# Performance work log

Hardware: AMD Instinct MI355X
Metric: run time of the kernel (lower is better)

The kernel has to match this reference:

```python
import jax, jax.numpy as jnp
import numpy as np

N_HEAD = 8
DROP_RATE = 0.1


def setup_inputs() -> dict:
    key = jax.random.key(0)
    k1, k2, k3 = jax.random.split(key, 3)
    n, c, h, w = 16, 512, 32, 32
    return {
        "x": jax.random.normal(k1, (n, c, h, w), jnp.float32),
        "qkv_w": jax.random.normal(k2, (3 * c, c), jnp.float32) * 0.02,
        "qkv_b": jnp.zeros((3 * c,), jnp.float32),
        "out_w": jax.random.normal(k3, (c, c), jnp.float32) * 0.02,
        "out_b": jnp.zeros((c,), jnp.float32),
        "dropout_enabled": 0,
    }


def reference(x, qkv_w, qkv_b, out_w, out_b, dropout_enabled):
    n, c, h, w = x.shape
    hd = c // N_HEAD  # head dim
    # fused QKV 1x1 conv == per-pixel matmul: [n, 3c, h, w]
    qkv = jnp.einsum('oc,nchw->nohw', qkv_w, x) + qkv_b[None, :, None, None]
    # [n, 3*n_head, hd, h*w] -> [n, 3*n_head, h*w, hd]
    qkv = jnp.swapaxes(qkv.reshape(n, N_HEAD * 3, hd, h * w), 2, 3)
    q, k, v = jnp.split(qkv, 3, axis=1)  # each [n, n_head, hw, hd]
    scale = hd ** (-0.25)
    att = jax.nn.softmax((q * scale) @ (jnp.swapaxes(k, 2, 3) * scale), axis=3)
    y = jnp.swapaxes(att @ v, 2, 3).reshape(n, c, h, w)
    y = jnp.einsum('oc,nchw->nohw', out_w, y) + out_b[None, :, None, None]
    # Dropout2d: drops whole (n, c) channel maps
    rate = DROP_RATE * dropout_enabled
    keep = jax.random.bernoulli(jax.random.key(42), 1.0 - rate, shape=(n, c))
    y = y * keep[..., None, None] / (1.0 - rate)
    return x + y
```

## Files before the change

### kernel.cpp

```cpp
#include <hip/hip_runtime.h>

typedef short bf16x8 __attribute__((ext_vector_type(8)));
typedef float f32x4 __attribute__((ext_vector_type(4)));
typedef float f32x16 __attribute__((ext_vector_type(16)));

#define MFMA16(a,b,c) __builtin_amdgcn_mfma_f32_16x16x32_bf16((a),(b),(c),0,0,0)
#define MFMA32(a,b,c) __builtin_amdgcn_mfma_f32_32x32x16_bf16((a),(b),(c),0,0,0)

static __device__ __forceinline__ unsigned short f2bf(float f){
  unsigned u; __builtin_memcpy(&u, &f, 4);
  u += 0x7fffu + ((u >> 16) & 1u);
  return (unsigned short)(u >> 16);
}

static __device__ __forceinline__ unsigned cvtpk(float lo, float hi){
  unsigned r;
  asm volatile("v_cvt_pk_bf16_f32 %0, %1, %2" : "=v"(r) : "v"(lo), "v"(hi));
  return r;
}
static __device__ __forceinline__ void pl32swap(unsigned &a, unsigned &b){
  asm volatile("v_permlane32_swap_b32 %0, %1" : "+v"(a), "+v"(b));
}

static __device__ __forceinline__ void gload_lds16(const void* g, void* l) {
  __builtin_amdgcn_global_load_lds(
      (__attribute__((address_space(1))) void*)g,
      (__attribute__((address_space(3))) void*)l, 16, 0, 0);
}

__global__ __launch_bounds__(256) void cvt_bf16(
    const float* __restrict__ in, unsigned short* __restrict__ out, int n) {
  int i = blockIdx.x * 256 + threadIdx.x;
  if (i < n) out[i] = f2bf(in[i]);
}

__global__ __launch_bounds__(256) void transpose_cvt(
    const float* __restrict__ in, unsigned short* __restrict__ out)
{
  __shared__ unsigned short tile[32][33];
  const long base = (long)blockIdx.z * 512 * 1024;
  const int t = threadIdx.x, tx = t & 31, ty = t >> 5;
  const int c0 = blockIdx.x * 32, r0 = blockIdx.y * 32;
  const float* ib = in + base;
#pragma unroll
  for (int i = 0; i < 4; ++i)
    tile[ty + i * 8][tx] = f2bf(ib[(long)(r0 + ty + i * 8) * 1024 + c0 + tx]);
  __syncthreads();
  unsigned short* ob = out + base;
#pragma unroll
  for (int i = 0; i < 4; ++i)
    ob[(long)(c0 + ty + i * 8) * 512 + r0 + tx] = tile[tx][ty + i * 8];
}

__global__ __launch_bounds__(256, 2) void gemm_qkv(
    const unsigned short* __restrict__ A, const unsigned short* __restrict__ B,
    unsigned short* __restrict__ qkvout, const float* __restrict__ bias)
{
  const int M = 1024, K = 512;
  __shared__ unsigned short SM[4][128 * 64];
  const int t = threadIdx.x, lane = t & 63, wv = t >> 6;
  const int quad = lane >> 4, ln = lane & 15;

  const int L = blockIdx.x + 12 * blockIdx.y + 96 * blockIdx.z;
  const int v = (L & 7) * 192 + (L >> 3);
  const int m0 = ((v / 12) & 7) * 128, n0 = (v % 12) * 128;
  const long zb = v / 96;
  A += zb * (long)M * K;

  const int srow = wv * 32 + (lane >> 3);
  const int scol = ((lane & 7) * 8) ^ ((lane >> 3) * 8);

  auto stage = [&](int kt, unsigned short* Ad, unsigned short* Bd) {
#pragma unroll
    for (int i = 0; i < 4; ++i) {
      gload_lds16(&A[(long)(m0 + srow + i * 8) * K + kt + scol],
                  &Ad[(wv * 32 + i * 8) * 64]);
      gload_lds16(&B[(long)(n0 + srow + i * 8) * K + kt + scol],
                  &Bd[(wv * 32 + i * 8) * 64]);
    }
  };

  f32x4 zero = {0.f, 0.f, 0.f, 0.f};
  f32x4 acc[4][4];
#pragma unroll
  for (int i = 0; i < 4; ++i)
#pragma unroll
    for (int j = 0; j < 4; ++j) acc[i][j] = zero;

  const int wm = (wv & 1) * 64, wn = (wv >> 1) * 64;
  const int rsw = (ln & 7) * 8;

  stage(0, SM[0], SM[2]);
  __syncthreads();
  for (int kt8 = 0; kt8 < 8; ++kt8) {
    const int cur = kt8 & 1;
    if (kt8 < 7) stage((kt8 + 1) * 64, SM[cur ^ 1], SM[2 + (cur ^ 1)]);
    const unsigned short* As = SM[cur];
    const unsigned short* Bs = SM[2 + cur];
#pragma unroll
    for (int kk = 0; kk < 64; kk += 32) {
      bf16x8 a[4], b[4];
#pragma unroll
      for (int i = 0; i < 4; ++i)
        a[i] = *(const bf16x8*)&As[(wm + i * 16 + ln) * 64 + ((kk + quad * 8) ^ rsw)];
#pragma unroll
      for (int j = 0; j < 4; ++j)
        b[j] = *(const bf16x8*)&Bs[(wn + j * 16 + ln) * 64 + ((kk + quad * 8) ^ rsw)];
#pragma unroll
      for (int i = 0; i < 4; ++i)
#pragma unroll
        for (int j = 0; j < 4; ++j)
          acc[i][j] = MFMA16(a[i], b[j], acc[i][j]);
    }
    __syncthreads();
  }

  const int part = n0 >> 9;
  if (part < 2) {
    const float qs = (part == 0) ? 0.18033688f : 1.0f;
    unsigned short (*T)[136] = (unsigned short(*)[136])&SM[0][0];
#pragma unroll
    for (int j = 0; j < 4; ++j) {
      const int oo = wn + j * 16 + ln;
      const float bb = bias[n0 + oo];
#pragma unroll
      for (int i = 0; i < 4; ++i) {
        const int pp = wm + i * 16 + quad * 4;
        f32x4 vv = acc[i][j];
#pragma unroll
        for (int r = 0; r < 4; ++r)
          T[pp + r][oo] = f2bf((vv[r] + bb) * qs);
      }
    }
    __syncthreads();
    unsigned short* qb = qkvout + (long)part * 8388608;
#pragma unroll
    for (int it = 0; it < 8; ++it) {
      const int idx = it * 256 + t;
      const int p = idx >> 4, c0 = (idx & 15) * 8;
      const int og = n0 + c0;
      const int h = (og >> 6) & 7, d = og & 63;
      bf16x8 val = *(const bf16x8*)&T[p][c0];
      *(bf16x8*)&qb[((long)(zb * 8 + h) * 1024 + m0 + p) * 64 + d] = val;
    }
  } else {
#pragma unroll
    for (int j = 0; j < 4; ++j) {
      const int o = n0 + wn + j * 16 + ln;
      const float bb = bias[o];
#pragma unroll
      for (int i = 0; i < 4; ++i) {
        const int p = m0 + wm + i * 16 + quad * 4;
        const long cidx = ((long)zb * 512 + (o - 1024)) * 1024 + p;
        f32x4 vv = acc[i][j];
        ushort4 st;
        st.x = f2bf(vv[0] + bb); st.y = f2bf(vv[1] + bb);
        st.z = f2bf(vv[2] + bb); st.w = f2bf(vv[3] + bb);
        *(ushort4*)&qkvout[16777216 + cidx] = st;
      }
    }
  }
}

__global__ __launch_bounds__(256, 2) void gemm_out(
    const unsigned short* __restrict__ A, const unsigned short* __restrict__ B,
    float* __restrict__ C, const float* __restrict__ bias,
    const float* __restrict__ xin, const int* __restrict__ de_ptr)
{
  const int M = 1024, K = 512;
  __shared__ unsigned short SM[4][128 * 64];
  const int t = threadIdx.x, lane = t & 63, wv = t >> 6;
  const int quad = lane >> 4, ln = lane & 15;

  const int L = blockIdx.x + 4 * blockIdx.y + 32 * blockIdx.z;
  const int v = (L & 7) * 64 + (L >> 3);
  const int m0 = ((v >> 2) & 7) * 128, n0 = (v & 3) * 128;
  const long zb = v >> 5;
  A += zb * (long)M * K;
  C += zb * 512l * M;
  xin += zb * 512l * M;

  const int srow = wv * 32 + (lane >> 3);
  const int scol = ((lane & 7) * 8) ^ ((lane >> 3) * 8);

  auto stage = [&](int kt, unsigned short* Ad, unsigned short* Bd) {
#pragma unroll
    for (int i = 0; i < 4; ++i) {
      gload_lds16(&A[(long)(m0 + srow + i * 8) * K + kt + scol],
                  &Ad[(wv * 32 + i * 8) * 64]);
      gload_lds16(&B[(long)(n0 + srow + i * 8) * K + kt + scol],
                  &Bd[(wv * 32 + i * 8) * 64]);
    }
  };

  f32x4 zero = {0.f, 0.f, 0.f, 0.f};
  f32x4 acc[4][4];
#pragma unroll
  for (int i = 0; i < 4; ++i)
#pragma unroll
    for (int j = 0; j < 4; ++j) acc[i][j] = zero;

  const int wm = (wv & 1) * 64, wn = (wv >> 1) * 64;
  const int rsw = (ln & 7) * 8;

  stage(0, SM[0], SM[2]);
  __syncthreads();
  for (int kt8 = 0; kt8 < 8; ++kt8) {
    const int cur = kt8 & 1;
    if (kt8 < 7) stage((kt8 + 1) * 64, SM[cur ^ 1], SM[2 + (cur ^ 1)]);
    const unsigned short* As = SM[cur];
    const unsigned short* Bs = SM[2 + cur];
#pragma unroll
    for (int kk = 0; kk < 64; kk += 32) {
      bf16x8 a[4], b[4];
#pragma unroll
      for (int i = 0; i < 4; ++i)
        a[i] = *(const bf16x8*)&As[(wm + i * 16 + ln) * 64 + ((kk + quad * 8) ^ rsw)];
#pragma unroll
      for (int j = 0; j < 4; ++j)
        b[j] = *(const bf16x8*)&Bs[(wn + j * 16 + ln) * 64 + ((kk + quad * 8) ^ rsw)];
#pragma unroll
      for (int i = 0; i < 4; ++i)
#pragma unroll
        for (int j = 0; j < 4; ++j)
          acc[i][j] = MFMA16(a[i], b[j], acc[i][j]);
    }
    __syncthreads();
  }

  float dscale = 1.0f / (1.0f - 0.1f * (float)de_ptr[0]);

#pragma unroll
  for (int j = 0; j < 4; ++j) {
    int o = n0 + wn + j * 16 + ln;
    float bb = bias[o];
#pragma unroll
    for (int i = 0; i < 4; ++i) {
      int p = m0 + wm + i * 16 + quad * 4;
      long cidx = (long)o * M + p;
      f32x4 vv = acc[i][j];
      float4 rx = *(const float4*)&xin[cidx];
      float4 st;
      st.x = rx.x + (vv[0] + bb) * dscale;
      st.y = rx.y + (vv[1] + bb) * dscale;
      st.z = rx.z + (vv[2] + bb) * dscale;
      st.w = rx.w + (vv[3] + bb) * dscale;
      *(float4*)&C[cidx] = st;
    }
  }
}

__global__ __launch_bounds__(256, 2) void attn_kernel(
    const unsigned short* __restrict__ q_pd, const unsigned short* __restrict__ k_pd,
    const unsigned short* __restrict__ v_cp, unsigned short* __restrict__ y_pc)
{
  __shared__ unsigned short Ks[2][128 * 64];
  __shared__ unsigned short Vs[2][64 * 128];
  const int t = threadIdx.x, lane = t & 63, wv = t >> 6;
  const int l31 = lane & 31, bh8 = (lane >> 5) * 8;
  const int qt = blockIdx.y >> 5;
  const int nh = blockIdx.x * 32 + (blockIdx.y & 31);
  const int n = nh >> 3, h = nh & 7;
  const int q0 = qt * 256;

  bf16x8 qa[2][4];
#pragma unroll
  for (int qg = 0; qg < 2; ++qg) {
    const unsigned short* qb =
        q_pd + ((long)nh * 1024 + q0 + wv * 64 + qg * 32 + l31) * 64;
#pragma unroll
    for (int ds = 0; ds < 4; ++ds)
      qa[qg][ds] = *(const bf16x8*)(qb + ds * 16 + bh8);
  }

  f32x16 zacc;
#pragma unroll
  for (int r = 0; r < 16; ++r) zacc[r] = 0.f;
  f32x16 o_acc[2][2];
  o_acc[0][0] = zacc; o_acc[0][1] = zacc; o_acc[1][0] = zacc; o_acc[1][1] = zacc;
  float l_acc[2] = {0.f, 0.f};

  const unsigned short* kg0 = k_pd + (long)nh * 1024 * 64;
  const unsigned short* vg0 = v_cp + ((long)n * 512 + h * 64) * 1024;

  const int krow = lane >> 3;
  const int kcol = ((lane & 7) * 8) ^ ((lane >> 3) * 8);
  const int vrow = lane >> 4;
  const int rsw = (lane & 7) * 8;
  const int vrsw = (l31 & 15) * 8;

#pragma unroll
  for (int i = 0; i < 4; ++i) {
    const int vr = i * 4 + vrow;
    const int vcol = ((lane & 15) ^ vr) * 8;
    gload_lds16(kg0 + (long)(wv * 32 + i * 8 + krow) * 64 + kcol,
                &Ks[0][(wv * 32 + i * 8) * 64]);
    gload_lds16(vg0 + (long)(wv * 16 + vr) * 1024 + vcol,
                &Vs[0][(wv * 16 + i * 4) * 128]);
  }
  __syncthreads();

  union U { bf16x8 v; unsigned u[4]; };
  auto sm_pack = [&](const f32x16& sv, bf16x8* paq, float& lac) {
    float e[16];
#pragma unroll
    for (int r = 0; r < 16; ++r) e[r] = __builtin_amdgcn_exp2f(sv[r]);
    float ls = 0.f;
#pragma unroll
    for (int r = 0; r < 16; ++r) ls += e[r];
    lac += ls;
    unsigned pk4[4][2];
#pragma unroll
    for (int hh = 0; hh < 4; ++hh) {
      pk4[hh][0] = cvtpk(e[4 * hh + 0], e[4 * hh + 1]);
      pk4[hh][1] = cvtpk(e[4 * hh + 2], e[4 * hh + 3]);
    }
#pragma unroll
    for (int hk = 0; hk < 2; ++hk) {
      unsigned a0 = pk4[2 * hk + 1][0], b0 = pk4[2 * hk][0];
      unsigned a1 = pk4[2 * hk + 1][1], b1 = pk4[2 * hk][1];
      pl32swap(a0, b0); pl32swap(a1, b1);
      U u; u.u[0] = b0; u.u[1] = b1; u.u[2] = a0; u.u[3] = a1;
      paq[hk] = u.v;
    }
  };

  for (int c = 0; c < 8; ++c) {
    const int cur = c & 1;
    if (c < 7) {
      const unsigned short* kg = kg0 + (long)(c + 1) * 128 * 64;
      const unsigned short* vg = vg0 + (c + 1) * 128;
      unsigned short* KsD = Ks[cur ^ 1];
      unsigned short* VsD = Vs[cur ^ 1];
#pragma unroll
      for (int i = 0; i < 4; ++i) {
        const int vr = i * 4 + vrow;
        const int vcol = ((lane & 15) ^ vr) * 8;
        gload_lds16(kg + (long)(wv * 32 + i * 8 + krow) * 64 + kcol,
                    &KsD[(wv * 32 + i * 8) * 64]);
        gload_lds16(vg + (long)(wv * 16 + vr) * 1024 + vcol,
                    &VsD[(wv * 16 + i * 4) * 128]);
      }
    }
    const unsigned short* KsC = Ks[cur];
    const unsigned short* VsC = Vs[cur];

#pragma unroll
    for (int kgi = 0; kgi < 4; ++kgi) {
      f32x16 s0 = zacc, s1 = zacc;
      __builtin_amdgcn_s_setprio(1);
#pragma unroll
      for (int ds = 0; ds < 4; ++ds) {
        bf16x8 ka = *(const bf16x8*)&KsC[(kgi * 32 + l31) * 64 + ((ds * 16 + bh8) ^ rsw)];
        s0 = MFMA32(ka, qa[0][ds], s0);
        s1 = MFMA32(ka, qa[1][ds], s1);
      }
      __builtin_amdgcn_s_setprio(0);
      bf16x8 pa[2][2];
      sm_pack(s0, pa[0], l_acc[0]);
      sm_pack(s1, pa[1], l_acc[1]);
      __builtin_amdgcn_s_setprio(1);
#pragma unroll
      for (int dg = 0; dg < 2; ++dg)
#pragma unroll
        for (int hk = 0; hk < 2; ++hk) {
          bf16x8 va = *(const bf16x8*)
              &VsC[(dg * 32 + l31) * 128 + (((kgi * 2 + hk) * 16 + bh8) ^ vrsw)];
          o_acc[dg][0] = MFMA32(va, pa[0][hk], o_acc[dg][0]);
          o_acc[dg][1] = MFMA32(va, pa[1][hk], o_acc[dg][1]);
        }
      __builtin_amdgcn_s_setprio(0);
    }
    __syncthreads();
  }

#pragma unroll
  for (int qg = 0; qg < 2; ++qg) {
    float la = l_acc[qg];
    la += __shfl_xor(la, 32);
    float linv = 1.0f / la;
    const int q = q0 + wv * 64 + qg * 32 + l31;
    unsigned short* yb = y_pc + ((long)n * 1024 + q) * 512 + h * 64;
#pragma unroll
    for (int dg = 0; dg < 2; ++dg) {
      f32x16 o = o_acc[dg][qg];
#pragma unroll
      for (int rq = 0; rq < 4; ++rq) {
        int d0 = dg * 32 + rq * 8 + (bh8 >> 1);
        ushort4 st;
        st.x = f2bf(o[rq * 4 + 0] * linv);
        st.y = f2bf(o[rq * 4 + 1] * linv);
        st.z = f2bf(o[rq * 4 + 2] * linv);
        st.w = f2bf(o[rq * 4 + 3] * linv);
        *(ushort4*)&yb[d0] = st;
      }
    }
  }
}

extern "C" void kernel_launch(void* const* d_in, const int* in_sizes, int n_in,
                              void* d_out, int out_size, void* d_ws, size_t ws_size,
                              hipStream_t stream) {
  (void)in_sizes; (void)n_in; (void)out_size; (void)ws_size;
  const float* x     = (const float*)d_in[0];
  const float* qkv_w = (const float*)d_in[1];
  const float* qkv_b = (const float*)d_in[2];
  const float* out_w = (const float*)d_in[3];
  const float* out_b = (const float*)d_in[4];
  const int* de = (const int*)d_in[5];
  float* out = (float*)d_out;
  unsigned short* ws = (unsigned short*)d_ws;

  unsigned short* xT   = ws;
  unsigned short* qkv  = ws + 8388608;
  unsigned short* y_pc = ws;
  unsigned short* wq   = ws + 33554432;
  unsigned short* wo   = wq + 786432;

  cvt_bf16<<<3072, 256, 0, stream>>>(qkv_w, wq, 786432);
  cvt_bf16<<<1024, 256, 0, stream>>>(out_w, wo, 262144);

  transpose_cvt<<<dim3(32, 16, 16), 256, 0, stream>>>(x, xT);

  gemm_qkv<<<dim3(12, 8, 16), 256, 0, stream>>>(xT, wq, qkv, qkv_b);

  attn_kernel<<<dim3(4, 128), 256, 0, stream>>>(
      qkv, qkv + 8388608, qkv + 16777216, y_pc);

  gemm_out<<<dim3(4, 8, 16), 256, 0, stream>>>(
      y_pc, wo, out, out_b, x, de);
}
```

Before: 186.0 us.

## Split attention query tile across eight waves of 32 queries each

The attention block grows from 256 to 512 threads. Each wave now owns 32 query rows instead of 64, and the K/V staging into shared memory is divided among the eight waves. The aim is to raise wave-level parallelism and cut per-wave accumulator registers to improve latency hiding. In exchange, each K/V fragment read from LDS feeds only one MFMA instead of two, which doubles LDS read traffic. The stricter launch bound also caps registers tightly and may cause spills, while LDS usage of 64KB per block still limits how many blocks fit per CU.

New measurement: 187.7 us. Within noise of the previous version (+0.9%).

```diff
diff --git a/kernel.cpp b/kernel.cpp
--- a/kernel.cpp
+++ b/kernel.cpp
@@ -250,7 +250,7 @@
   }
 }
 
-__global__ __launch_bounds__(256, 2) void attn_kernel(
+__global__ __launch_bounds__(512, 4) void attn_kernel(
     const unsigned short* __restrict__ q_pd, const unsigned short* __restrict__ k_pd,
     const unsigned short* __restrict__ v_cp, unsigned short* __restrict__ y_pc)
 {
@@ -263,22 +263,21 @@
   const int n = nh >> 3, h = nh & 7;
   const int q0 = qt * 256;
 
-  bf16x8 qa[2][4];
-#pragma unroll
-  for (int qg = 0; qg < 2; ++qg) {
+  bf16x8 qa[4];
+  {
     const unsigned short* qb =
-        q_pd + ((long)nh * 1024 + q0 + wv * 64 + qg * 32 + l31) * 64;
+        q_pd + ((long)nh * 1024 + q0 + wv * 32 + l31) * 64;
 #pragma unroll
     for (int ds = 0; ds < 4; ++ds)
-      qa[qg][ds] = *(const bf16x8*)(qb + ds * 16 + bh8);
+      qa[ds] = *(const bf16x8*)(qb + ds * 16 + bh8);
   }
 
   f32x16 zacc;
 #pragma unroll
   for (int r = 0; r < 16; ++r) zacc[r] = 0.f;
-  f32x16 o_acc[2][2];
-  o_acc[0][0] = zacc; o_acc[0][1] = zacc; o_acc[1][0] = zacc; o_acc[1][1] = zacc;
-  float l_acc[2] = {0.f, 0.f};
+  f32x16 o_acc[2];
+  o_acc[0] = zacc; o_acc[1] = zacc;
+  float l_acc = 0.f;
 
   const unsigned short* kg0 = k_pd + (long)nh * 1024 * 64;
   const unsigned short* vg0 = v_cp + ((long)n * 512 + h * 64) * 1024;
@@ -289,26 +288,31 @@
   const int rsw = (lane & 7) * 8;
   const int vrsw = (l31 & 15) * 8;
 
-#pragma unroll
-  for (int i = 0; i < 4; ++i) {
-    const int vr = i * 4 + vrow;
-    const int vcol = ((lane & 15) ^ vr) * 8;
-    gload_lds16(kg0 + (long)(wv * 32 + i * 8 + krow) * 64 + kcol,
-                &Ks[0][(wv * 32 + i * 8) * 64]);
-    gload_lds16(vg0 + (long)(wv * 16 + vr) * 1024 + vcol,
-                &Vs[0][(wv * 16 + i * 4) * 128]);
-  }
+  auto stage_kv = [&](const unsigned short* kg, const unsigned short* vg,
+                      unsigned short* KsD, unsigned short* VsD) {
+#pragma unroll
+    for (int i = 0; i < 2; ++i) {
+      const int vr = ((wv & 1) * 8) + i * 4 + vrow;
+      const int vcol = ((lane & 15) ^ vr) * 8;
+      gload_lds16(kg + (long)(wv * 16 + i * 8 + krow) * 64 + kcol,
+                  &KsD[(wv * 16 + i * 8) * 64]);
+      gload_lds16(vg + (long)(wv * 8 + i * 4 + vrow) * 1024 + vcol,
+                  &VsD[(wv * 8 + i * 4) * 128]);
+    }
+  };
+
+  stage_kv(kg0, vg0, Ks[0], Vs[0]);
   __syncthreads();
 
   union U { bf16x8 v; unsigned u[4]; };
-  auto sm_pack = [&](const f32x16& sv, bf16x8* paq, float& lac) {
+  auto sm_pack = [&](const f32x16& sv, bf16x8* paq) {
     float e[16];
 #pragma unroll
     for (int r = 0; r < 16; ++r) e[r] = __builtin_amdgcn_exp2f(sv[r]);
     float ls = 0.f;
 #pragma unroll
     for (int r = 0; r < 16; ++r) ls += e[r];
-    lac += ls;
+    l_acc += ls;
     unsigned pk4[4][2];
 #pragma unroll
     for (int hh = 0; hh < 4; ++hh) {
@@ -327,38 +331,24 @@
 
   for (int c = 0; c < 8; ++c) {
     const int cur = c & 1;
-    if (c < 7) {
-      const unsigned short* kg = kg0 + (long)(c + 1) * 128 * 64;
-      const unsigned short* vg = vg0 + (c + 1) * 128;
-      unsigned short* KsD = Ks[cur ^ 1];
-      unsigned short* VsD = Vs[cur ^ 1];
-#pragma unroll
-      for (int i = 0; i < 4; ++i) {
-        const int vr = i * 4 + vrow;
-        const int vcol = ((lane & 15) ^ vr) * 8;
-        gload_lds16(kg + (long)(wv * 32 + i * 8 + krow) * 64 + kcol,
-                    &KsD[(wv * 32 + i * 8) * 64]);
-        gload_lds16(vg + (long)(wv * 16 + vr) * 1024 + vcol,
-                    &VsD[(wv * 16 + i * 4) * 128]);
-      }
-    }
+    if (c < 7)
+      stage_kv(kg0 + (long)(c + 1) * 128 * 64, vg0 + (c + 1) * 128,
+               Ks[cur ^ 1], Vs[cur ^ 1]);
     const unsigned short* KsC = Ks[cur];
     const unsigned short* VsC = Vs[cur];
 
 #pragma unroll
     for (int kgi = 0; kgi < 4; ++kgi) {
-      f32x16 s0 = zacc, s1 = zacc;
+      f32x16 s = zacc;
       __builtin_amdgcn_s_setprio(1);
 #pragma unroll
       for (int ds = 0; ds < 4; ++ds) {
         bf16x8 ka = *(const bf16x8*)&KsC[(kgi * 32 + l31) * 64 + ((ds * 16 + bh8) ^ rsw)];
-        s0 = MFMA32(ka, qa[0][ds], s0);
-        s1 = MFMA32(ka, qa[1][ds], s1);
+        s = MFMA32(ka, qa[ds], s);
       }
       __builtin_amdgcn_s_setprio(0);
-      bf16x8 pa[2][2];
-      sm_pack(s0, pa[0], l_acc[0]);
-      sm_pack(s1, pa[1], l_acc[1]);
+      bf16x8 pa[2];
+      sm_pack(s, pa);
       __builtin_amdgcn_s_setprio(1);
 #pragma unroll
       for (int dg = 0; dg < 2; ++dg)
@@ -366,24 +356,22 @@
         for (int hk = 0; hk < 2; ++hk) {
           bf16x8 va = *(const bf16x8*)
               &VsC[(dg * 32 + l31) * 128 + (((kgi * 2 + hk) * 16 + bh8) ^ vrsw)];
-          o_acc[dg][0] = MFMA32(va, pa[0][hk], o_acc[dg][0]);
-          o_acc[dg][1] = MFMA32(va, pa[1][hk], o_acc[dg][1]);
+          o_acc[dg] = MFMA32(va, pa[hk], o_acc[dg]);
         }
       __builtin_amdgcn_s_setprio(0);
     }
     __syncthreads();
   }
 
-#pragma unroll
-  for (int qg = 0; qg < 2; ++qg) {
-    float la = l_acc[qg];
+  {
+    float la = l_acc;
     la += __shfl_xor(la, 32);
     float linv = 1.0f / la;
-    const int q = q0 + wv * 64 + qg * 32 + l31;
+    const int q = q0 + wv * 32 + l31;
     unsigned short* yb = y_pc + ((long)n * 1024 + q) * 512 + h * 64;
 #pragma unroll
     for (int dg = 0; dg < 2; ++dg) {
-      f32x16 o = o_acc[dg][qg];
+      f32x16 o = o_acc[dg];
 #pragma unroll
       for (int rq = 0; rq < 4; ++rq) {
         int d0 = dg * 32 + rq * 8 + (bh8 >> 1);
@@ -424,7 +412,7 @@
 
   gemm_qkv<<<dim3(12, 8, 16), 256, 0, stream>>>(xT, wq, qkv, qkv_b);
 
-  attn_kernel<<<dim3(4, 128), 256, 0, stream>>>(
+  attn_kernel<<<dim3(4, 128), 512, 0, stream>>>(
       qkv, qkv + 8388608, qkv + 16777216, y_pc);
 
   gemm_out<<<dim3(4, 8, 16), 256, 0, stream>>>(
```

## Triple-buffer attention K/V with 512-thread blocks and split-wait pipelining in GEMMs

Applied to the files above, without the earlier changes.

The attention kernel moves to 512-thread blocks that each cover 512 queries, with K/V staging split across 8 waves. It triple-buffers the K/V tiles in LDS and prefetches two chunks ahead, using explicit vmcnt waits and raw barriers in place of full __syncthreads. Both GEMMs replace __syncthreads with a partial vmcnt wait plus s_barrier so the next tile's loads stay in flight, and the two weight-conversion launches are merged into one. The intent is more load/compute overlap and fewer launches, at the cost of more LDS per block (96KB), which may reduce occupancy. The hand-written vmcnt counts must match the number of outstanding loads exactly or reads become unsafe.

Result: slower. 198.8 us (+6.8%).

```diff
diff --git a/kernel.cpp b/kernel.cpp
--- a/kernel.cpp
+++ b/kernel.cpp
@@ -28,10 +28,12 @@
       (__attribute__((address_space(3))) void*)l, 16, 0, 0);
 }
 
-__global__ __launch_bounds__(256) void cvt_bf16(
-    const float* __restrict__ in, unsigned short* __restrict__ out, int n) {
+__global__ __launch_bounds__(256) void cvt_w(
+    const float* __restrict__ qkv_w, const float* __restrict__ out_w,
+    unsigned short* __restrict__ wq, unsigned short* __restrict__ wo) {
   int i = blockIdx.x * 256 + threadIdx.x;
-  if (i < n) out[i] = f2bf(in[i]);
+  if (i < 786432) wq[i] = f2bf(qkv_w[i]);
+  else            wo[i - 786432] = f2bf(out_w[i - 786432]);
 }
 
 __global__ __launch_bounds__(256) void transpose_cvt(
@@ -91,10 +93,15 @@
   const int rsw = (ln & 7) * 8;
 
   stage(0, SM[0], SM[2]);
-  __syncthreads();
   for (int kt8 = 0; kt8 < 8; ++kt8) {
     const int cur = kt8 & 1;
-    if (kt8 < 7) stage((kt8 + 1) * 64, SM[cur ^ 1], SM[2 + (cur ^ 1)]);
+    if (kt8 < 7) {
+      stage((kt8 + 1) * 64, SM[cur ^ 1], SM[2 + (cur ^ 1)]);
+      asm volatile("s_waitcnt vmcnt(8)" ::: "memory");
+    } else {
+      asm volatile("s_waitcnt vmcnt(0)" ::: "memory");
+    }
+    __builtin_amdgcn_s_barrier();
     const unsigned short* As = SM[cur];
     const unsigned short* Bs = SM[2 + cur];
 #pragma unroll
@@ -112,13 +119,14 @@
         for (int j = 0; j < 4; ++j)
           acc[i][j] = MFMA16(a[i], b[j], acc[i][j]);
     }
-    __syncthreads();
+    __builtin_amdgcn_s_barrier();
   }
 
   const int part = n0 >> 9;
   if (part < 2) {
     const float qs = (part == 0) ? 0.18033688f : 1.0f;
     unsigned short (*T)[136] = (unsigned short(*)[136])&SM[0][0];
+    __syncthreads();
 #pragma unroll
     for (int j = 0; j < 4; ++j) {
       const int oo = wn + j * 16 + ln;
@@ -204,10 +212,15 @@
   const int rsw = (ln & 7) * 8;
 
   stage(0, SM[0], SM[2]);
-  __syncthreads();
   for (int kt8 = 0; kt8 < 8; ++kt8) {
     const int cur = kt8 & 1;
-    if (kt8 < 7) stage((kt8 + 1) * 64, SM[cur ^ 1], SM[2 + (cur ^ 1)]);
+    if (kt8 < 7) {
+      stage((kt8 + 1) * 64, SM[cur ^ 1], SM[2 + (cur ^ 1)]);
+      asm volatile("s_waitcnt vmcnt(8)" ::: "memory");
+    } else {
+      asm volatile("s_waitcnt vmcnt(0)" ::: "memory");
+    }
+    __builtin_amdgcn_s_barrier();
     const unsigned short* As = SM[cur];
     const unsigned short* Bs = SM[2 + cur];
 #pragma unroll
@@ -225,7 +238,7 @@
         for (int j = 0; j < 4; ++j)
           acc[i][j] = MFMA16(a[i], b[j], acc[i][j]);
     }
-    __syncthreads();
+    __builtin_amdgcn_s_barrier();
   }
 
   float dscale = 1.0f / (1.0f - 0.1f * (float)de_ptr[0]);
@@ -250,18 +263,18 @@
   }
 }
 
-__global__ __launch_bounds__(256, 2) void attn_kernel(
+__global__ __launch_bounds__(512, 2) void attn_kernel(
     const unsigned short* __restrict__ q_pd, const unsigned short* __restrict__ k_pd,
     const unsigned short* __restrict__ v_cp, unsigned short* __restrict__ y_pc)
 {
-  __shared__ unsigned short Ks[2][128 * 64];
-  __shared__ unsigned short Vs[2][64 * 128];
+  __shared__ unsigned short Ks[3][128 * 64];
+  __shared__ unsigned short Vs[3][64 * 128];
   const int t = threadIdx.x, lane = t & 63, wv = t >> 6;
   const int l31 = lane & 31, bh8 = (lane >> 5) * 8;
   const int qt = blockIdx.y >> 5;
   const int nh = blockIdx.x * 32 + (blockIdx.y & 31);
   const int n = nh >> 3, h = nh & 7;
-  const int q0 = qt * 256;
+  const int q0 = qt * 512;
 
   bf16x8 qa[2][4];
 #pragma unroll
@@ -289,16 +302,24 @@
   const int rsw = (lane & 7) * 8;
   const int vrsw = (l31 & 15) * 8;
 
-#pragma unroll
-  for (int i = 0; i < 4; ++i) {
-    const int vr = i * 4 + vrow;
-    const int vcol = ((lane & 15) ^ vr) * 8;
-    gload_lds16(kg0 + (long)(wv * 32 + i * 8 + krow) * 64 + kcol,
-                &Ks[0][(wv * 32 + i * 8) * 64]);
-    gload_lds16(vg0 + (long)(wv * 16 + vr) * 1024 + vcol,
-                &Vs[0][(wv * 16 + i * 4) * 128]);
-  }
-  __syncthreads();
+  auto stage_kv = [&](int c, int buf) {
+    const unsigned short* kg = kg0 + (long)c * 128 * 64;
+    const unsigned short* vg = vg0 + c * 128;
+    unsigned short* KsD = Ks[buf];
+    unsigned short* VsD = Vs[buf];
+#pragma unroll
+    for (int i = 0; i < 2; ++i) {
+      const int vr = ((wv & 1) * 8) + i * 4 + vrow;
+      const int vcol = ((lane & 15) ^ vr) * 8;
+      gload_lds16(kg + (long)(wv * 16 + i * 8 + krow) * 64 + kcol,
+                  &KsD[(wv * 16 + i * 8) * 64]);
+      gload_lds16(vg + (long)(wv * 8 + i * 4 + vrow) * 1024 + vcol,
+                  &VsD[(wv * 8 + i * 4) * 128]);
+    }
+  };
+
+  stage_kv(0, 0);
+  stage_kv(1, 1);
 
   union U { bf16x8 v; unsigned u[4]; };
   auto sm_pack = [&](const f32x16& sv, bf16x8* paq, float& lac) {
@@ -326,22 +347,16 @@
   };
 
   for (int c = 0; c < 8; ++c) {
-    const int cur = c & 1;
-    if (c < 7) {
-      const unsigned short* kg = kg0 + (long)(c + 1) * 128 * 64;
-      const unsigned short* vg = vg0 + (c + 1) * 128;
-      unsigned short* KsD = Ks[cur ^ 1];
-      unsigned short* VsD = Vs[cur ^ 1];
-#pragma unroll
-      for (int i = 0; i < 4; ++i) {
-        const int vr = i * 4 + vrow;
-        const int vcol = ((lane & 15) ^ vr) * 8;
-        gload_lds16(kg + (long)(wv * 32 + i * 8 + krow) * 64 + kcol,
-                    &KsD[(wv * 32 + i * 8) * 64]);
-        gload_lds16(vg + (long)(wv * 16 + vr) * 1024 + vcol,
-                    &VsD[(wv * 16 + i * 4) * 128]);
-      }
-    }
+    const int cur = c % 3;
+    if (c < 6) {
+      stage_kv(c + 2, (c + 2) % 3);
+      asm volatile("s_waitcnt vmcnt(8)" ::: "memory");
+    } else if (c == 6) {
+      asm volatile("s_waitcnt vmcnt(4)" ::: "memory");
+    } else {
+      asm volatile("s_waitcnt vmcnt(0)" ::: "memory");
+    }
+    __builtin_amdgcn_s_barrier();
     const unsigned short* KsC = Ks[cur];
     const unsigned short* VsC = Vs[cur];
 
@@ -371,7 +386,7 @@
         }
       __builtin_amdgcn_s_setprio(0);
     }
-    __syncthreads();
+    __builtin_amdgcn_s_barrier();
   }
 
 #pragma unroll
@@ -417,14 +432,13 @@
   unsigned short* wq   = ws + 33554432;
   unsigned short* wo   = wq + 786432;
 
-  cvt_bf16<<<3072, 256, 0, stream>>>(qkv_w, wq, 786432);
-  cvt_bf16<<<1024, 256, 0, stream>>>(out_w, wo, 262144);
+  cvt_w<<<4096, 256, 0, stream>>>(qkv_w, out_w, wq, wo);
 
   transpose_cvt<<<dim3(32, 16, 16), 256, 0, stream>>>(x, xT);
 
   gemm_qkv<<<dim3(12, 8, 16), 256, 0, stream>>>(xT, wq, qkv, qkv_b);
 
-  attn_kernel<<<dim3(4, 128), 256, 0, stream>>>(
+  attn_kernel<<<dim3(4, 64), 512, 0, stream>>>(
       qkv, qkv + 8388608, qkv + 16777216, y_pc);
 
   gemm_out<<<dim3(4, 8, 16), 256, 0, stream>>>(
```
